# Optimization experiments

Hardware: AMD Instinct MI355X
Metric: run time of the kernel (lower is better)

## Reference

```python
import jax, jax.numpy as jnp
import numpy as np


def _ln(x, g, b, eps=1e-5):
    m = x.mean(-1, keepdims=True)
    v = ((x - m) ** 2).mean(-1, keepdims=True)
    return (x - m) / jnp.sqrt(v + eps) * g + b


def _conv(x, w, b, stride, pad, groups):
    # x: NCHW, w: OIHW (I = in_ch/groups)
    out = jax.lax.conv_general_dilated(
        x, w, (stride, stride), [(pad, pad), (pad, pad)],
        dimension_numbers=('NCHW', 'OIHW', 'NCHW'), feature_group_count=groups)
    return out + b[None, :, None, None]


def _gelu(x):
    return jax.nn.gelu(x, approximate=False)  # torch nn.GELU (exact erf)


def _forward(x, H, W, lpu_w, lpu_b, n1_g, n1_b, conv2d_w, conv2d_b, cn_g, cn_b,
             q_w, sr1_w, sr1_b, an1_g, an1_b, sr2_w, sr2_b, an2_g, an2_b,
             kv1_w, kv2_w, proj_w, proj_b, n2_g, n2_b,
             fc1_w, fc1_b, dw_w, dw_b, fc2_w, fc2_b):
    B, N, C = x.shape
    cd = C // 4          # conv_part_dim = 64
    ad = C - cd          # attn_part_dim = 192
    nh = 8
    hg = nh // 2         # heads per group
    hd = ad // nh        # head_dim = 24
    scale = hd ** -0.5
    # ---- LPU: depthwise 3x3 conv residual ----
    xi = x.transpose(0, 2, 1).reshape(B, C, H, W)
    xi = _conv(xi, lpu_w, lpu_b, 1, 1, C) + xi
    x = xi.reshape(B, C, N).transpose(0, 2, 1)
    # ---- Attention branch (pre-LN) ----
    y = _ln(x, n1_g, n1_b)
    cp, ap = y[..., :cd], y[..., cd:]
    # conv part: dense 3x3 conv (sr_ratio==8 -> kernel 3, pad 1), then LN+GELU in NLC
    cp = cp.reshape(B, H, W, cd).transpose(0, 3, 1, 2)
    cp = _conv(cp, conv2d_w, conv2d_b, 1, 1, 1).reshape(B, cd, N).transpose(0, 2, 1)
    cp = _gelu(_ln(cp, cn_g, cn_b))
    # attn part: dual spatial-reduction KV paths
    q = (ap @ q_w.T).reshape(B, N, nh, hd).transpose(0, 2, 1, 3)  # [B,nh,N,hd]
    x_ = ap.transpose(0, 2, 1).reshape(B, ad, H, W)
    x1 = _conv(x_, sr1_w, sr1_b, 8, 0, ad).reshape(B, ad, -1).transpose(0, 2, 1)  # [B,(H/8)(W/8),ad]
    x1 = _gelu(_ln(x1, an1_g, an1_b))
    x2 = _conv(x_, sr2_w, sr2_b, 4, 0, ad).reshape(B, ad, -1).transpose(0, 2, 1)  # [B,(H/4)(W/4),ad]
    x2 = _gelu(_ln(x2, an2_g, an2_b))
    kv1 = (x1 @ kv1_w.T).reshape(B, -1, 2, hg, hd).transpose(2, 0, 3, 1, 4)  # [2,B,hg,M1,hd]
    kv2 = (x2 @ kv2_w.T).reshape(B, -1, 2, hg, hd).transpose(2, 0, 3, 1, 4)

    def attn(qh, k, v):
        a = jax.nn.softmax(jnp.einsum('bhnd,bhmd->bhnm', qh, k) * scale, axis=-1)
        o = jnp.einsum('bhnm,bhmd->bhnd', a, v)
        return o.transpose(0, 2, 1, 3).reshape(B, N, -1)

    o1 = attn(q[:, :hg], kv1[0], kv1[1])
    o2 = attn(q[:, hg:], kv2[0], kv2[1])
    y = jnp.concatenate([o1, o2, cp], axis=-1) @ proj_w.T + proj_b
    x = x + y
    # ---- MLP with depthwise conv ----
    z = _ln(x, n2_g, n2_b) @ fc1_w.T + fc1_b
    hidc = z.shape[-1]
    z = z.transpose(0, 2, 1).reshape(B, hidc, H, W)
    z = _conv(z, dw_w, dw_b, 1, 1, hidc).reshape(B, hidc, N).transpose(0, 2, 1)
    z = _gelu(z) @ fc2_w.T + fc2_b
    return x + z


def setup_inputs() -> dict:
    key = jax.random.key(0)
    ks = jax.random.split(key, 16)
    B, H, W, C = 16, 56, 56, 256
    N = H * W
    cd, ad = C // 4, C * 3 // 4
    hid = 4 * C
    f = lambda i, shape, s=0.02: jax.random.normal(ks[i], shape, jnp.float32) * s
    return dict(
        x=jax.random.normal(ks[0], (B, N, C), jnp.float32),
        H=H, W=W,
        lpu_w=f(1, (C, 1, 3, 3), 0.1), lpu_b=jnp.zeros((C,), jnp.float32),
        n1_g=jnp.ones((C,), jnp.float32), n1_b=jnp.zeros((C,), jnp.float32),
        conv2d_w=f(2, (cd, cd, 3, 3), 0.05), conv2d_b=jnp.zeros((cd,), jnp.float32),
        cn_g=jnp.ones((cd,), jnp.float32), cn_b=jnp.zeros((cd,), jnp.float32),
        q_w=f(3, (ad, ad)),
        sr1_w=f(4, (ad, 1, 8, 8), 0.1), sr1_b=jnp.zeros((ad,), jnp.float32),
        an1_g=jnp.ones((ad,), jnp.float32), an1_b=jnp.zeros((ad,), jnp.float32),
        sr2_w=f(5, (ad, 1, 4, 4), 0.1), sr2_b=jnp.zeros((ad,), jnp.float32),
        an2_g=jnp.ones((ad,), jnp.float32), an2_b=jnp.zeros((ad,), jnp.float32),
        kv1_w=f(6, (ad, ad)), kv2_w=f(7, (ad, ad)),
        proj_w=f(8, (C, C)), proj_b=jnp.zeros((C,), jnp.float32),
        n2_g=jnp.ones((C,), jnp.float32), n2_b=jnp.zeros((C,), jnp.float32),
        fc1_w=f(9, (hid, C)), fc1_b=jnp.zeros((hid,), jnp.float32),
        dw_w=f(10, (hid, 1, 3, 3), 0.1), dw_b=jnp.zeros((hid,), jnp.float32),
        fc2_w=f(11, (C, hid)), fc2_b=jnp.zeros((C,), jnp.float32),
    )


def reference(x, H, W, lpu_w, lpu_b, n1_g, n1_b, conv2d_w, conv2d_b, cn_g, cn_b,
              q_w, sr1_w, sr1_b, an1_g, an1_b, sr2_w, sr2_b, an2_g, an2_b,
              kv1_w, kv2_w, proj_w, proj_b, n2_g, n2_b,
              fc1_w, fc1_b, dw_w, dw_b, fc2_w, fc2_b):
    return _forward(x, H, W, lpu_w, lpu_b, n1_g, n1_b, conv2d_w, conv2d_b, cn_g, cn_b,
                    q_w, sr1_w, sr1_b, an1_g, an1_b, sr2_w, sr2_b, an2_g, an2_b,
                    kv1_w, kv2_w, proj_w, proj_b, n2_g, n2_b,
                    fc1_w, fc1_b, dw_w, dw_b, fc2_w, fc2_b)
```

## Files before the change

kernel.cpp:

```cpp
#include <hip/hip_runtime.h>
#include <math.h>

#define BB   16
#define HH   56
#define WW   56
#define NN   (HH*WW)
#define CC   256
#define CD   64
#define AD   192
#define NH   8
#define HG   4
#define HD   24
#define HID  1024
#define M1   49
#define M2   196
#define BNR  (BB*NN)

typedef __attribute__((ext_vector_type(8))) short s8v;
typedef __attribute__((ext_vector_type(4))) short s4v;
typedef __attribute__((ext_vector_type(4))) float f4v;
typedef __attribute__((ext_vector_type(8))) _Float16 h8v;
typedef __attribute__((ext_vector_type(2))) _Float16 h2v;

__device__ __forceinline__ float gelu_f(float x) {
    float u = x * (1.0f + 0.044715f * x * x);
    float t = __expf(-1.5957691216f * u);
    return x * __builtin_amdgcn_rcpf(1.0f + t);
}
__device__ __forceinline__ ushort f2bf(float f) {
    union { float f; uint32_t u; } c; c.f = f;
    uint32_t u = c.u;
    return (ushort)((u + 0x7fffu + ((u >> 16) & 1u)) >> 16);
}
__device__ __forceinline__ float bf2f(ushort u) {
    union { uint32_t u; float f; } c; c.u = ((uint32_t)u) << 16;
    return c.f;
}
__device__ __forceinline__ ushort f2h(float f) {
    union { _Float16 h; ushort u; } c; c.h = (_Float16)f;
    return c.u;
}
__device__ __forceinline__ void load_lds16(const void* gsrc, void* ldst) {
    __builtin_amdgcn_global_load_lds(
        (const __attribute__((address_space(1))) void*)gsrc,
        (__attribute__((address_space(3))) void*)ldst, 16, 0, 0);
}
__device__ __forceinline__ int xcd_swz(int bid, int nwg) {
    int q = nwg >> 3, r = nwg & 7;
    int x = bid & 7, i = bid >> 3;
    return (x < r ? x * (q + 1) : r * (q + 1) + (x - r) * q) + i;
}

__global__ __launch_bounds__(256) void wprep_kernel(
        const float* __restrict__ qw, const float* __restrict__ k1,
        const float* __restrict__ k2, const float* __restrict__ pw,
        const float* __restrict__ f1, const float* __restrict__ f2,
        const float* __restrict__ cw, const float* __restrict__ lw,
        const float* __restrict__ dw,
        ushort* __restrict__ wq, ushort* __restrict__ wkv1,
        ushort* __restrict__ wkv2, ushort* __restrict__ wpr,
        ushort* __restrict__ wf1, ushort* __restrict__ wf2,
        ushort* __restrict__ wcp, float* __restrict__ lpwt,
        ushort* __restrict__ dwwth) {
    int i = blockIdx.x * 256 + threadIdx.x;
    if (i < 36864) { wq[i] = f2bf(qw[i]); return; } i -= 36864;
    if (i < 36864) { wkv1[i] = f2bf(k1[i]); return; } i -= 36864;
    if (i < 36864) { wkv2[i] = f2bf(k2[i]); return; } i -= 36864;
    if (i < 65536) { wpr[i] = f2bf(pw[i]); return; } i -= 65536;
    if (i < 262144) { wf1[i] = f2bf(f1[i]); return; } i -= 262144;
    if (i < 262144) { wf2[i] = f2h(f2[i]); return; } i -= 262144;
    if (i < 36864) {
        int co = i / 576, k = i - co * 576;
        int tap = k >> 6, ci = k & 63;
        wcp[i] = f2bf(cw[co * 576 + ci * 9 + tap]);
        return;
    } i -= 36864;
    if (i < 2304) { int c = i / 9, t = i - c * 9; lpwt[t * CC + c] = lw[i]; return; } i -= 2304;
    if (i < 9216) { int c = i / 9, t = i - c * 9; dwwth[t * HID + c] = f2h(dw[i]); }
}

__global__ __launch_bounds__(256) void lpu_kernel(const float* __restrict__ x,
        const float* __restrict__ wt, const float* __restrict__ bias,
        const float* __restrict__ n1g, const float* __restrict__ n1b,
        ushort* __restrict__ xbuf, ushort* __restrict__ ybuf) {
    int tid = threadIdx.x;
    int lane = tid & 63, wv = tid >> 6;
    int c = lane * 4;
    int grp = xcd_swz(blockIdx.x, NN / 16) * 4 + wv;
    int n0 = grp * 4;
    int h = n0 / WW, x0 = n0 - h * WW;
    int b = blockIdx.y;
    const float* xb = x + (size_t)b * NN * CC + c;
    float4 wreg[9];
#pragma unroll
    for (int t = 0; t < 9; ++t) wreg[t] = *(const float4*)(wt + t * CC + c);
    float4 bz = *(const float4*)(bias + c);
    float4 acc[4] = {bz, bz, bz, bz};
#pragma unroll
    for (int cx = 0; cx < 6; ++cx) {
        int wx = x0 + cx - 1;
        if ((unsigned)wx >= (unsigned)WW) continue;
#pragma unroll
        for (int ky = 0; ky < 3; ++ky) {
            int hy = h + ky - 1;
            if ((unsigned)hy >= (unsigned)HH) continue;
            float4 xv = *(const float4*)(xb + (size_t)(hy * WW + wx) * CC);
#pragma unroll
            for (int xo = 0; xo < 4; ++xo) {
                int kx = cx - xo;
                if (kx < 0 || kx > 2) continue;
                float4 wv4 = wreg[ky * 3 + kx];
                acc[xo].x = fmaf(xv.x, wv4.x, acc[xo].x);
                acc[xo].y = fmaf(xv.y, wv4.y, acc[xo].y);
                acc[xo].z = fmaf(xv.z, wv4.z, acc[xo].z);
                acc[xo].w = fmaf(xv.w, wv4.w, acc[xo].w);
            }
        }
    }
    float4 gv = *(const float4*)(n1g + c);
    float4 bv = *(const float4*)(n1b + c);
#pragma unroll
    for (int xo = 0; xo < 4; ++xo) {
        size_t o = ((size_t)b * NN + n0 + xo) * CC + c;
        float4 rv = *(const float4*)(x + o);
        float4 a = acc[xo];
        a.x += rv.x; a.y += rv.y; a.z += rv.z; a.w += rv.w;
        s4v xv4;
        xv4.x = (short)f2bf(a.x);
        xv4.y = (short)f2bf(a.y);
        xv4.z = (short)f2bf(a.z);
        xv4.w = (short)f2bf(a.w);
        *(s4v*)(xbuf + o) = xv4;
        float s = a.x + a.y + a.z + a.w;
        float sq = a.x * a.x + a.y * a.y + a.z * a.z + a.w * a.w;
#pragma unroll
        for (int off = 32; off >= 1; off >>= 1) {
            s += __shfl_xor(s, off, 64);
            sq += __shfl_xor(sq, off, 64);
        }
        float mean = s * (1.0f / 256.0f);
        float var = sq * (1.0f / 256.0f) - mean * mean;
        float rstd = rsqrtf(var + 1e-5f);
        s4v ov;
        ov.x = (short)f2bf((a.x - mean) * rstd * gv.x + bv.x);
        ov.y = (short)f2bf((a.y - mean) * rstd * gv.y + bv.y);
        ov.z = (short)f2bf((a.z - mean) * rstd * gv.z + bv.z);
        ov.w = (short)f2bf((a.w - mean) * rstd * gv.w + bv.w);
        *(s4v*)(ybuf + o) = ov;
    }
}

__device__ __forceinline__ void cpgemm_body(
        const ushort* __restrict__ y, const ushort* __restrict__ wt,
        const float* __restrict__ cb, const float* __restrict__ cng,
        const float* __restrict__ cnb, ushort* __restrict__ cat,
        ushort* As , ushort* Ws , int tile) {
    int tid = threadIdx.x;
    int wid = tid >> 6, lane = tid & 63;
    int rt = xcd_swz(tile, BNR / 128) * 128;
    int r0 = tid >> 2, c0 = tid & 3;
    int r1 = r0 + 64;
    int tok0 = rt + r0, tok1 = rt + r1;
    int b0 = tok0 / NN, n0 = tok0 - b0 * NN, h0 = n0 / WW, w0 = n0 - h0 * WW;
    int b1 = tok1 / NN, n1 = tok1 - b1 * NN, h1 = n1 / WW, w1 = n1 - h1 * WW;
    const ushort* Wp = wt + (size_t)r0 * 576 + c0 * 8;
    int aw0 = (c0 ^ (r0 & 3)) << 3;
    f4v acc[2][4];
#pragma unroll
    for (int m = 0; m < 2; ++m)
#pragma unroll
        for (int n = 0; n < 4; ++n) acc[m][n] = (f4v)0.f;
    int lr = lane & 15, g4 = lane >> 4;
    int swz = (g4 ^ (lr & 3)) << 3;
    for (int kt = 0; kt < 576; kt += 32) {
        int tap = kt >> 6, ci0 = kt & 63;
        int t3 = tap / 3, dy = t3 - 1, dx = (tap - t3 * 3) - 1;
        s8v a0 = (s8v)0, a1 = (s8v)0;
        int hy0 = h0 + dy, wx0 = w0 + dx;
        if ((unsigned)hy0 < (unsigned)HH && (unsigned)wx0 < (unsigned)WW)
            a0 = *(const s8v*)(y + ((size_t)b0 * NN + hy0 * WW + wx0) * CC + ci0 + c0 * 8);
        int hy1 = h1 + dy, wx1 = w1 + dx;
        if ((unsigned)hy1 < (unsigned)HH && (unsigned)wx1 < (unsigned)WW)
            a1 = *(const s8v*)(y + ((size_t)b1 * NN + hy1 * WW + wx1) * CC + ci0 + c0 * 8);
        s8v wv = *(const s8v*)(Wp + kt);
        __syncthreads();
        *(s8v*)&As[r0 * 32 + aw0] = a0;
        *(s8v*)&As[r1 * 32 + aw0] = a1;
        *(s8v*)&Ws[r0 * 32 + aw0] = wv;
        __syncthreads();
        s8v af[2], bf[4];
#pragma unroll
        for (int m = 0; m < 2; ++m)
            af[m] = *(const s8v*)&As[(wid * 32 + m * 16 + lr) * 32 + swz];
#pragma unroll
        for (int n = 0; n < 4; ++n)
            bf[n] = *(const s8v*)&Ws[(n * 16 + lr) * 32 + swz];
#pragma unroll
        for (int m = 0; m < 2; ++m)
#pragma unroll
            for (int n = 0; n < 4; ++n)
                acc[m][n] = __builtin_amdgcn_mfma_f32_16x16x32_bf16(af[m], bf[n], acc[m][n], 0, 0, 0);
    }
    float gv[4], bv[4], cbv[4];
#pragma unroll
    for (int n = 0; n < 4; ++n) {
        int gc = n * 16 + lr;
        cbv[n] = cb[gc];
        gv[n] = cng[gc];
        bv[n] = cnb[gc];
    }
#pragma unroll
    for (int m = 0; m < 2; ++m)
#pragma unroll
        for (int r = 0; r < 4; ++r) {
            float s = 0.f, sq = 0.f;
#pragma unroll
            for (int n = 0; n < 4; ++n) {
                float v = acc[m][n][r] + cbv[n];
                acc[m][n][r] = v;
                s += v; sq += v * v;
            }
#pragma unroll
            for (int off = 1; off < 16; off <<= 1) {
                s += __shfl_xor(s, off, 64);
                sq += __shfl_xor(sq, off, 64);
            }
            float mean = s * (1.0f / 64.0f);
            float var = sq * (1.0f / 64.0f) - mean * mean;
            float rstd = rsqrtf(var + 1e-5f);
            int row = rt + wid * 32 + m * 16 + g4 * 4 + r;
            ushort* op = cat + (size_t)row * CC + 192;
#pragma unroll
            for (int n = 0; n < 4; ++n) {
                float v = (acc[m][n][r] - mean) * rstd * gv[n] + bv[n];
                op[n * 16 + lr] = f2bf(gelu_f(v));
            }
        }
}

template <int KS, int OW>
__device__ __forceinline__ void sr_body(const ushort* __restrict__ yap,
        const float* __restrict__ w, const float* __restrict__ bias,
        const float* __restrict__ g, const float* __restrict__ bt,
        ushort* __restrict__ out, int m, int b) {
    int ch = threadIdx.x;
    int oh = m / OW, ow = m - oh * OW;
    const ushort* yb = yap + (size_t)b * NN * CC;
    float acc = bias[ch];
#pragma unroll
    for (int ky = 0; ky < KS; ++ky)
#pragma unroll
        for (int kx = 0; kx < KS; ++kx)
            acc = fmaf(bf2f(yb[(size_t)((oh * KS + ky) * WW + ow * KS + kx) * CC + ch]),
                       w[ch * KS * KS + ky * KS + kx], acc);
    __shared__ float red[2][3];
    float s = acc, sq = acc * acc;
#pragma unroll
    for (int off = 32; off >= 1; off >>= 1) {
        s += __shfl_xor(s, off, 64);
        sq += __shfl_xor(sq, off, 64);
    }
    int wv = threadIdx.x >> 6, lane = threadIdx.x & 63;
    if (lane == 0) { red[0][wv] = s; red[1][wv] = sq; }
    __syncthreads();
    s = red[0][0] + red[0][1] + red[0][2];
    sq = red[1][0] + red[1][1] + red[1][2];
    float mean = s * (1.0f / 192.0f);
    float var = sq * (1.0f / 192.0f) - mean * mean;
    float rstd = rsqrtf(var + 1e-5f);
    float v = (acc - mean) * rstd * g[ch] + bt[ch];
    out[((size_t)b * (OW * OW) + m) * AD + ch] = f2bf(gelu_f(v));
}

__global__ __launch_bounds__(192) void sr_both(const ushort* __restrict__ yap,
        const float* __restrict__ w1, const float* __restrict__ b1,
        const float* __restrict__ g1, const float* __restrict__ t1,
        ushort* __restrict__ o1,
        const float* __restrict__ w2, const float* __restrict__ b2,
        const float* __restrict__ g2, const float* __restrict__ t2,
        ushort* __restrict__ o2) {
    int b = blockIdx.y;
    if (blockIdx.x < M2) sr_body<4, 14>(yap, w2, b2, g2, t2, o2, blockIdx.x, b);
    else                 sr_body<8, 7>(yap, w1, b1, g1, t1, o1, blockIdx.x - M2, b);
}

template <int MODE, int F16>
__device__ __forceinline__ void gemm_body(
        const ushort* __restrict__ A, int lda,
        const ushort* __restrict__ W, int K, int O,
        const float* __restrict__ bias,
        const ushort* __restrict__ res, int ldr,
        void* __restrict__ Cout, int ldc, int R,
        int gx, int nwg, int bid) {
    __shared__ __align__(16) ushort As[2 * 256 * 32];
    __shared__ __align__(16) ushort Ws[2 * 128 * 32];
    int tid = threadIdx.x;
    int w8 = tid >> 6, lane = tid & 63;
    int wr = w8 >> 1, wc = w8 & 1;
    int swzb = xcd_swz(bid, nwg);
    int rt = (swzb / gx) * 256, ot = (swzb % gx) * 128;
    int r0 = tid >> 2, cslot = tid & 3;
    int csrc = (cslot ^ (r0 & 3)) * 8;
    const ushort* Ap0 = A + (size_t)min(rt + r0, R - 1) * lda + csrc;
    const ushort* Ap1 = A + (size_t)min(rt + r0 + 128, R - 1) * lda + csrc;
    const ushort* Wp0 = W + (size_t)min(ot + r0, O - 1) * K + csrc;
    char* lA0 = (char*)As + w8 * 1024;
    char* lA1 = (char*)As + 8192 + w8 * 1024;
    char* lW0 = (char*)Ws + w8 * 1024;
    f4v acc[4][4];
#pragma unroll
    for (int m = 0; m < 4; ++m)
#pragma unroll
        for (int n = 0; n < 4; ++n) acc[m][n] = (f4v)0.f;
    int lr = lane & 15;
    int swz = ((lane >> 4) ^ (lr & 3)) << 3;
    load_lds16(Ap0, lA0);
    load_lds16(Ap1, lA1);
    load_lds16(Wp0, lW0);
    __syncthreads();
    int cur = 0;
    for (int kt = 0; kt < K; kt += 32) {
        if (kt + 32 < K) {
            int pa = (cur ^ 1) * 16384, pw = (cur ^ 1) * 8192;
            load_lds16(Ap0 + kt + 32, lA0 + pa);
            load_lds16(Ap1 + kt + 32, lA1 + pa);
            load_lds16(Wp0 + kt + 32, lW0 + pw);
        }
        const ushort* Ab = As + cur * 8192;
        const ushort* Wb = Ws + cur * 4096;
        s8v af[4], bf[4];
#pragma unroll
        for (int m = 0; m < 4; ++m)
            af[m] = *(const s8v*)&Ab[(wr * 64 + m * 16 + lr) * 32 + swz];
#pragma unroll
        for (int n = 0; n < 4; ++n)
            bf[n] = *(const s8v*)&Wb[(wc * 64 + n * 16 + lr) * 32 + swz];
#pragma unroll
        for (int m = 0; m < 4; ++m)
#pragma unroll
            for (int n = 0; n < 4; ++n) {
                if (F16) {
                    h8v ah = *(const h8v*)&af[m];
                    h8v bh = *(const h8v*)&bf[n];
                    acc[m][n] = __builtin_amdgcn_mfma_f32_16x16x32_f16(ah, bh, acc[m][n], 0, 0, 0);
                } else {
                    acc[m][n] = __builtin_amdgcn_mfma_f32_16x16x32_bf16(af[m], bf[n], acc[m][n], 0, 0, 0);
                }
            }
        __syncthreads();
        cur ^= 1;
    }
#pragma unroll
    for (int m = 0; m < 4; ++m)
#pragma unroll
        for (int n = 0; n < 4; ++n) {
            int gr = rt + wr * 64 + m * 16 + (lane >> 4) * 4;
            int gc = ot + wc * 64 + n * 16 + (lane & 15);
            if (gc >= O) continue;
#pragma unroll
            for (int r = 0; r < 4; ++r) {
                int row = gr + r;
                if (row >= R) continue;
                float v = acc[m][n][r];
                if (MODE & 1) v += bias[gc];
                if (MODE & 2) v += bf2f(res[(size_t)row * ldr + gc]);
                if (MODE & 4)      ((ushort*)Cout)[(size_t)row * ldc + gc] = f2bf(v);
                else if (MODE & 8) ((ushort*)Cout)[(size_t)row * ldc + gc] = f2h(v);
                else               ((float*)Cout)[(size_t)row * ldc + gc] = v;
            }
        }
}

__global__ __launch_bounds__(512) void kvq_all(
        const ushort* __restrict__ yap, const ushort* __restrict__ wq,
        ushort* __restrict__ qbuf,
        const ushort* __restrict__ x1g, const ushort* __restrict__ wkv1,
        ushort* __restrict__ kv1b,
        const ushort* __restrict__ x2g, const ushort* __restrict__ wkv2,
        ushort* __restrict__ kv2b) {
    int bid = blockIdx.y * 2 + blockIdx.x;
    if (blockIdx.z == 0) {
        gemm_body<4, 0>(yap, CC, wq, AD, AD, nullptr, nullptr, 0,
                        qbuf, AD, BNR, 2, 392, bid);
    } else if (blockIdx.z == 1) {
        if (blockIdx.y >= 4) return;
        gemm_body<4, 0>(x1g, AD, wkv1, AD, AD, nullptr, nullptr, 0,
                        kv1b, AD, BB * M1, 2, 8, bid);
    } else {
        if (blockIdx.y >= 13) return;
        gemm_body<4, 0>(x2g, AD, wkv2, AD, AD, nullptr, nullptr, 0,
                        kv2b, AD, BB * M2, 2, 26, bid);
    }
}

template <int MODE, int F16 = 0>
__global__ __launch_bounds__(1024) void gemm_8ph(
        const ushort* __restrict__ A, int lda,
        const ushort* __restrict__ W, int K, int O,
        const float* __restrict__ bias,
        const ushort* __restrict__ res, int ldr,
        void* __restrict__ Cout, int ldc, int R) {
    __shared__ __align__(16) ushort Al[2 * 256 * 64];
    __shared__ __align__(16) ushort Wl[2 * 256 * 64];
    int tid = threadIdx.x;
    int w16 = tid >> 6, lane = tid & 63;
    int wr = w16 >> 2, wc = w16 & 3;
    int nwg = gridDim.x * gridDim.y;
    int swzb = xcd_swz(blockIdx.y * gridDim.x + blockIdx.x, nwg);
    int rt = (swzb / gridDim.x) * 256, ot = (swzb % gridDim.x) * 256;
    int lr = lane & 15, g4 = lane >> 4;
    int swz = (g4 ^ (lr & 3)) << 3;
    int ar0 = tid >> 2, sp0 = tid & 3;
    int cs0 = ((sp0 ^ (ar0 & 3)) << 3);
    const ushort* Ap0 = A + (size_t)(rt + ar0) * lda + cs0;
    const ushort* Wp0 = W + (size_t)(ot + ar0) * K + cs0;
    int d0 = w16 * 1024;
    f4v acc[4][4];
#pragma unroll
    for (int m = 0; m < 4; ++m)
#pragma unroll
        for (int n = 0; n < 4; ++n)
            acc[m][n] = (f4v)((MODE & 1) ? bias[ot + wc * 64 + n * 16 + lr] : 0.0f);
    auto STAGE = [&](int s) {
        int t = s >> 1, hf = s & 1;
        int boff = (t & 1) * 32768 + hf * 16384;
        int kc = t * 64 + hf * 32;
        load_lds16(Ap0 + kc, (char*)Al + boff + d0);
        load_lds16(Wp0 + kc, (char*)Wl + boff + d0);
    };
    int nS = K >> 5;
    STAGE(0); STAGE(1); STAGE(2);
    for (int s = 0; s < nS; ++s) {
        if (s < nS - 2)       asm volatile("s_waitcnt vmcnt(4)" ::: "memory");
        else if (s == nS - 2) asm volatile("s_waitcnt vmcnt(2)" ::: "memory");
        else                  asm volatile("s_waitcnt vmcnt(0)" ::: "memory");
        __builtin_amdgcn_s_barrier();
        __builtin_amdgcn_sched_barrier(0);
        if (s + 3 < nS) STAGE(s + 3);
        int uoff = ((s >> 1) & 1) * 16384 + (s & 1) * 8192;
        const ushort* Ab = Al + uoff;
        const ushort* Wb = Wl + uoff;
        s8v af[4], bf[4];
#pragma unroll
        for (int m = 0; m < 4; ++m)
            af[m] = *(const s8v*)&Ab[(wr * 64 + m * 16 + lr) * 32 + swz];
#pragma unroll
        for (int n = 0; n < 4; ++n)
            bf[n] = *(const s8v*)&Wb[(wc * 64 + n * 16 + lr) * 32 + swz];
        __builtin_amdgcn_s_setprio(1);
#pragma unroll
        for (int m = 0; m < 4; ++m)
#pragma unroll
            for (int n = 0; n < 4; ++n) {
                if (F16) {
                    h8v ah = *(const h8v*)&af[m];
                    h8v bh = *(const h8v*)&bf[n];
                    acc[m][n] = __builtin_amdgcn_mfma_f32_16x16x32_f16(ah, bh, acc[m][n], 0, 0, 0);
                } else {
                    acc[m][n] = __builtin_amdgcn_mfma_f32_16x16x32_bf16(af[m], bf[n], acc[m][n], 0, 0, 0);
                }
            }
        __builtin_amdgcn_s_setprio(0);
    }
#pragma unroll
    for (int m = 0; m < 4; ++m) {
        int gr = rt + wr * 64 + m * 16 + g4 * 4;
#pragma unroll
        for (int n = 0; n < 4; ++n) {
            int gc = ot + wc * 64 + n * 16 + lr;
#pragma unroll
            for (int r = 0; r < 4; ++r) {
                int row = gr + r;
                float v = acc[m][n][r];
                if (MODE & 2) v += bf2f(res[(size_t)row * ldr + gc]);
                if (MODE & 4)      ((ushort*)Cout)[(size_t)row * ldc + gc] = f2bf(v);
                else if (MODE & 8) ((ushort*)Cout)[(size_t)row * ldc + gc] = f2h(v);
                else               ((float*)Cout)[(size_t)row * ldc + gc] = v;
            }
        }
    }
}

__global__ __launch_bounds__(512) void projln_kernel(
        const ushort* __restrict__ A, const ushort* __restrict__ W,
        const float* __restrict__ bias,
        const float* __restrict__ n2g, const float* __restrict__ n2b,
        ushort* __restrict__ xbuf, ushort* __restrict__ ybuf) {
    __shared__ __align__(16) ushort As[128 * 32];
    __shared__ __align__(16) ushort Ws[256 * 32];
    int tid = threadIdx.x;
    int w8 = tid >> 6, lane = tid & 63;
    int rt = xcd_swz(blockIdx.x, BNR / 128) * 128;
    int r0 = tid >> 2, cslot = tid & 3;
    int csrc = (cslot ^ (r0 & 3)) * 8;
    const ushort* Ap0 = A + (size_t)(rt + r0) * CC + csrc;
    const ushort* Wp0 = W + (size_t)r0 * CC + csrc;
    const ushort* Wp1 = W + (size_t)(r0 + 128) * CC + csrc;
    char* lA0 = (char*)As + w8 * 1024;
    char* lW0 = (char*)Ws + w8 * 1024;
    char* lW1 = (char*)Ws + 8192 + w8 * 1024;
    int lr = lane & 15, g4 = lane >> 4;
    int swz = (g4 ^ (lr & 3)) << 3;
    f4v acc[16];
#pragma unroll
    for (int n = 0; n < 16; ++n) acc[n] = (f4v)(bias[n * 16 + lr]);
    for (int kt = 0; kt < CC; kt += 32) {
        __syncthreads();
        load_lds16(Ap0 + kt, lA0);
        load_lds16(Wp0 + kt, lW0);
        load_lds16(Wp1 + kt, lW1);
        __syncthreads();
        s8v af = *(const s8v*)&As[(w8 * 16 + lr) * 32 + swz];
#pragma unroll
        for (int n = 0; n < 16; ++n) {
            s8v bf = *(const s8v*)&Ws[(n * 16 + lr) * 32 + swz];
            acc[n] = __builtin_amdgcn_mfma_f32_16x16x32_bf16(af, bf, acc[n], 0, 0, 0);
        }
    }
#pragma unroll
    for (int r = 0; r < 4; ++r) {
        int row = rt + w8 * 16 + g4 * 4 + r;
        ushort* xr = xbuf + (size_t)row * CC;
        ushort* yr = ybuf + (size_t)row * CC;
        float s = 0.f, sq = 0.f;
#pragma unroll
        for (int n = 0; n < 16; ++n) {
            float v = acc[n][r] + bf2f(xr[n * 16 + lr]);
            acc[n][r] = v;
            s += v; sq += v * v;
        }
#pragma unroll
        for (int off = 1; off < 16; off <<= 1) {
            s += __shfl_xor(s, off, 64);
            sq += __shfl_xor(sq, off, 64);
        }
        float mean = s * (1.0f / 256.0f);
        float var = sq * (1.0f / 256.0f) - mean * mean;
        float rstd = rsqrtf(var + 1e-5f);
#pragma unroll
        for (int n = 0; n < 16; ++n) {
            int col = n * 16 + lr;
            float v = acc[n][r];
            xr[col] = f2bf(v);
            yr[col] = f2bf((v - mean) * rstd * n2g[col] + n2b[col]);
        }
    }
}

template <int M, int MP>
__device__ __forceinline__ void attn_body(const ushort* __restrict__ q,
        const ushort* __restrict__ kvb, ushort* __restrict__ cat,
        ushort* Kl, ushort* VT, int g, int h, int b) {
    constexpr int NT = MP / 16;
    constexpr int NCH = MP / 32;
    int tid = threadIdx.x;
    for (int i = tid; i < MP * 4; i += 256) ((s8v*)Kl)[i] = (s8v)0;
    for (int i = tid; i < MP * 4; i += 256) ((s8v*)VT)[i] = (s8v)0;
    __syncthreads();
    for (int u = tid; u < M * 3; u += 256) {
        int m = u / 3, d0 = u - m * 3;
        s8v kv8 = *(const s8v*)(kvb + ((size_t)b * M + m) * AD + g * HD + d0 * 8);
        *(s8v*)&Kl[m * 32 + ((d0 ^ (m & 3)) << 3)] = kv8;
    }
    for (int u = tid; u < M * 3; u += 256) {
        int m = u / 3, d0 = u - m * 3;
        s8v vv = *(const s8v*)(kvb + ((size_t)b * M + m) * AD + 96 + g * HD + d0 * 8);
        int c = m >> 5, mm = m & 31;
        int gg = (mm >> 2) & 3;
        int t = (mm & 3) + ((mm & 16) >> 2);
#pragma unroll
        for (int j = 0; j < 8; ++j) {
            int d = d0 * 8 + j;
            VT[d * MP + ((c * 4 + (gg ^ (d & 3))) << 3) + t] = (ushort)vv[j];
        }
    }
    __syncthreads();
    int w = tid >> 6, lane = tid & 63;
    int ln = lane & 15, g4 = lane >> 4;
    int swz = (g4 ^ (ln & 3)) << 3;
    const float scale = 0.20412414523193154f;
    for (int nt = 0; nt < 4; ++nt) {
        int nbase = blockIdx.x * 256 + nt * 64;
        if (nbase >= NN) break;
        int n0 = nbase + w * 16 + ln;
        s8v qf = (s8v)0;
        if (g4 < 3) qf = *(const s8v*)(q + ((size_t)b * NN + n0) * AD + h * HD + g4 * 8);
        f4v sa[NT];
#pragma unroll
        for (int t = 0; t < NT; ++t) sa[t] = (f4v)0.f;
#pragma unroll
        for (int t = 0; t < NT; ++t) {
            s8v kf = *(const s8v*)&Kl[(t * 16 + ln) * 32 + swz];
            sa[t] = __builtin_amdgcn_mfma_f32_16x16x32_bf16(kf, qf, sa[t], 0, 0, 0);
        }
        float mx = -3.0e38f;
#pragma unroll
        for (int t = 0; t < NT; ++t)
#pragma unroll
            for (int r = 0; r < 4; ++r) {
                int m = t * 16 + g4 * 4 + r;
                float v = (m < M) ? sa[t][r] * scale : -3.0e38f;
                sa[t][r] = v;
                mx = fmaxf(mx, v);
            }
        mx = fmaxf(mx, __shfl_xor(mx, 16, 64));
        mx = fmaxf(mx, __shfl_xor(mx, 32, 64));
        float sum = 0.f;
#pragma unroll
        for (int t = 0; t < NT; ++t)
#pragma unroll
            for (int r = 0; r < 4; ++r) {
                float p = __expf(sa[t][r] - mx);
                sa[t][r] = p;
                sum += p;
            }
        sum += __shfl_xor(sum, 16, 64);
        sum += __shfl_xor(sum, 32, 64);
        float inv = 1.0f / sum;
        f4v oa[2] = {(f4v)0.f, (f4v)0.f};
#pragma unroll
        for (int c = 0; c < NCH; ++c) {
            s8v pb;
#pragma unroll
            for (int t = 0; t < 4; ++t) {
                pb[t]     = (short)f2bf(sa[c * 2][t]);
                pb[4 + t] = (short)f2bf(sa[c * 2 + 1][t]);
            }
#pragma unroll
            for (int dt = 0; dt < 2; ++dt) {
                s8v vf = *(const s8v*)&VT[(dt * 16 + ln) * MP + c * 32 + swz];
                oa[dt] = __builtin_amdgcn_mfma_f32_16x16x32_bf16(vf, pb, oa[dt], 0, 0, 0);
            }
        }
        ushort* op = cat + ((size_t)b * NN + n0) * CC + h * HD;
        s4v o0;
#pragma unroll
        for (int r = 0; r < 4; ++r) o0[r] = (short)f2bf(oa[0][r] * inv);
        *(s4v*)(op + g4 * 4) = o0;
        if (g4 < 2) {
            s4v o1;
#pragma unroll
            for (int r = 0; r < 4; ++r) o1[r] = (short)f2bf(oa[1][r] * inv);
            *(s4v*)(op + 16 + g4 * 4) = o1;
        }
    }
}

__global__ __launch_bounds__(256) void attn_both(const ushort* __restrict__ q,
        const ushort* __restrict__ kv1b, const ushort* __restrict__ kv2b,
        ushort* __restrict__ cat,
        const ushort* __restrict__ ybuf, const ushort* __restrict__ wcp,
        const float* __restrict__ cb, const float* __restrict__ cng,
        const float* __restrict__ cnb) {
    __shared__ __align__(16) ushort Kl[224 * 32];
    __shared__ __align__(16) ushort VT[32 * 224];
    int hy = blockIdx.y, b = blockIdx.z;
    if (hy < HG)      attn_body<M1, 64>(q, kv1b, cat, Kl, VT, hy, hy, b);
    else if (hy < NH) attn_body<M2, 224>(q, kv2b, cat, Kl, VT, hy - HG, hy, b);
    else {
        int id = blockIdx.x + 13 * blockIdx.z;
        for (int t = id * 2; t < id * 2 + 2; ++t)
            if (t < BNR / 128)
                cpgemm_body(ybuf, wcp, cb, cng, cnb, cat, Kl, VT, t);
    }
}

__global__ __launch_bounds__(256) void dwconv_kernel(const ushort* __restrict__ z1,
        const ushort* __restrict__ wt, const float* __restrict__ bias,
        ushort* __restrict__ z2) {
    int bid = xcd_swz(blockIdx.x, HH * 7);
    int h = bid / 7, bx = bid - h * 7;
    int b = blockIdx.y;
    int c = (threadIdx.x & 127) * 8;
    int x0 = bx * 8 + (threadIdx.x >> 7) * 4;
    const ushort* zrow = z1 + ((size_t)b * NN + h * WW) * HID + c;
    h2v wreg[9][4];
#pragma unroll
    for (int t = 0; t < 9; ++t) {
        s8v w8 = *(const s8v*)(wt + t * HID + c);
        const h2v* wp = (const h2v*)&w8;
#pragma unroll
        for (int p = 0; p < 4; ++p) wreg[t][p] = wp[p];
    }
    h2v acc[4][4];
    {
        float4 b0 = *(const float4*)(bias + c);
        float4 b1 = *(const float4*)(bias + c + 4);
        h2v bz[4];
        bz[0][0] = (_Float16)b0.x; bz[0][1] = (_Float16)b0.y;
        bz[1][0] = (_Float16)b0.z; bz[1][1] = (_Float16)b0.w;
        bz[2][0] = (_Float16)b1.x; bz[2][1] = (_Float16)b1.y;
        bz[3][0] = (_Float16)b1.z; bz[3][1] = (_Float16)b1.w;
#pragma unroll
        for (int xo = 0; xo < 4; ++xo)
#pragma unroll
            for (int p = 0; p < 4; ++p) acc[xo][p] = bz[p];
    }
#pragma unroll
    for (int cx = 0; cx < 6; ++cx) {
        int wx = x0 + cx - 1;
        if ((unsigned)wx >= (unsigned)WW) continue;
#pragma unroll
        for (int ky = 0; ky < 3; ++ky) {
            int hy = h + ky - 1;
            if ((unsigned)hy >= (unsigned)HH) continue;
            s8v v = *(const s8v*)(zrow + ((size_t)(ky - 1) * WW + wx) * HID);
            const h2v* v2 = (const h2v*)&v;
#pragma unroll
            for (int xo = 0; xo < 4; ++xo) {
                int kx = cx - xo;
                if (kx < 0 || kx > 2) continue;
#pragma unroll
                for (int p = 0; p < 4; ++p)
                    acc[xo][p] = v2[p] * wreg[ky * 3 + kx][p] + acc[xo][p];
            }
        }
    }
    ushort* zo = z2 + ((size_t)b * NN + h * WW + x0) * HID + c;
#pragma unroll
    for (int xo = 0; xo < 4; ++xo) {
        s8v o;
#pragma unroll
        for (int p = 0; p < 4; ++p) {
            o[p * 2]     = (short)f2h(gelu_f((float)acc[xo][p][0]));
            o[p * 2 + 1] = (short)f2h(gelu_f((float)acc[xo][p][1]));
        }
        *(s8v*)(zo + (size_t)xo * HID) = o;
    }
}

extern "C" void kernel_launch(void* const* d_in, const int* in_sizes, int n_in,
                              void* d_out, int out_size, void* d_ws, size_t ws_size,
                              hipStream_t stream) {
    const float* x      = (const float*)d_in[0];
    const float* lpu_w  = (const float*)d_in[3];
    const float* lpu_b  = (const float*)d_in[4];
    const float* n1_g   = (const float*)d_in[5];
    const float* n1_b   = (const float*)d_in[6];
    const float* c2_w   = (const float*)d_in[7];
    const float* c2_b   = (const float*)d_in[8];
    const float* cn_g   = (const float*)d_in[9];
    const float* cn_b   = (const float*)d_in[10];
    const float* q_w    = (const float*)d_in[11];
    const float* sr1_w  = (const float*)d_in[12];
    const float* sr1_b  = (const float*)d_in[13];
    const float* an1_g  = (const float*)d_in[14];
    const float* an1_b  = (const float*)d_in[15];
    const float* sr2_w  = (const float*)d_in[16];
    const float* sr2_b  = (const float*)d_in[17];
    const float* an2_g  = (const float*)d_in[18];
    const float* an2_b  = (const float*)d_in[19];
    const float* kv1_w  = (const float*)d_in[20];
    const float* kv2_w  = (const float*)d_in[21];
    const float* proj_w = (const float*)d_in[22];
    const float* proj_b = (const float*)d_in[23];
    const float* n2_g   = (const float*)d_in[24];
    const float* n2_b   = (const float*)d_in[25];
    const float* fc1_w  = (const float*)d_in[26];
    const float* fc1_b  = (const float*)d_in[27];
    const float* dw_w   = (const float*)d_in[28];
    const float* dw_b   = (const float*)d_in[29];
    const float* fc2_w  = (const float*)d_in[30];
    const float* fc2_b  = (const float*)d_in[31];
    float* out = (float*)d_out;

    char* ws = (char*)d_ws;
    size_t off = 0;
    auto allocB = [&](size_t bytes) {
        char* p = ws + off;
        off += ((bytes + 255) & ~(size_t)255);
        return p;
    };
    ushort* xbuf = (ushort*)allocB((size_t)BNR * CC * 2);
    ushort* ybuf = (ushort*)allocB((size_t)BNR * CC * 2);
    ushort* wq   = (ushort*)allocB((size_t)AD * AD * 2);
    ushort* wkv1 = (ushort*)allocB((size_t)AD * AD * 2);
    ushort* wkv2 = (ushort*)allocB((size_t)AD * AD * 2);
    ushort* wpr  = (ushort*)allocB((size_t)CC * CC * 2);
    ushort* wf1  = (ushort*)allocB((size_t)HID * CC * 2);
    ushort* wf2  = (ushort*)allocB((size_t)CC * HID * 2);
    ushort* wcp  = (ushort*)allocB((size_t)64 * 576 * 2);
    float*  lpwt = (float*)allocB((size_t)9 * CC * 4);
    ushort* dwwt = (ushort*)allocB((size_t)9 * HID * 2);
    size_t zmark = off;
    ushort* cat  = (ushort*)allocB((size_t)BNR * CC * 2);
    ushort* qbuf = (ushort*)allocB((size_t)BNR * AD * 2);
    ushort* x1g  = (ushort*)allocB((size_t)BB * M1 * AD * 2);
    ushort* x2g  = (ushort*)allocB((size_t)BB * M2 * AD * 2);
    ushort* kv1b = (ushort*)allocB((size_t)BB * M1 * AD * 2);
    ushort* kv2b = (ushort*)allocB((size_t)BB * M2 * AD * 2);

    int CB2 = 1;
    for (int cb = 16; cb >= 1; cb >>= 1) {
        if (zmark + 2 * (size_t)cb * NN * HID * 2 <= ws_size) { CB2 = cb; break; }
    }

    dim3 b256(256), b512(512), b1024(1024);
    wprep_kernel<<<dim3(2925), b256, 0, stream>>>(
        q_w, kv1_w, kv2_w, proj_w, fc1_w, fc2_w, c2_w, lpu_w, dw_w,
        wq, wkv1, wkv2, wpr, wf1, wf2, wcp, lpwt, dwwt);
    lpu_kernel<<<dim3(NN / 16, BB), b256, 0, stream>>>(x, lpwt, lpu_b, n1_g, n1_b, xbuf, ybuf);
    sr_both<<<dim3(M1 + M2, BB), dim3(192), 0, stream>>>(ybuf + CD,
        sr1_w, sr1_b, an1_g, an1_b, x1g, sr2_w, sr2_b, an2_g, an2_b, x2g);
    kvq_all<<<dim3(2, 196, 3), b512, 0, stream>>>(
        ybuf + CD, wq, qbuf, x1g, wkv1, kv1b, x2g, wkv2, kv2b);
    attn_both<<<dim3((NN + 255) / 256, NH + 1, BB), b256, 0, stream>>>(
        qbuf, kv1b, kv2b, cat, ybuf, wcp, c2_b, cn_g, cn_b);
    projln_kernel<<<dim3(BNR / 128), b512, 0, stream>>>(
        cat, wpr, proj_b, n2_g, n2_b, xbuf, ybuf);
    ushort* z1 = (ushort*)(ws + zmark);
    ushort* z2 = z1 + (size_t)CB2 * NN * HID;
    for (int c0 = 0; c0 < BB; c0 += CB2) {
        size_t tokoff = (size_t)c0 * NN;
        int Rr = CB2 * NN;
        gemm_8ph<9><<<dim3(HID / 256, Rr / 256), b1024, 0, stream>>>(
            ybuf + tokoff * CC, CC, wf1, CC, HID, fc1_b, nullptr, 0, z1, HID, Rr);
        dwconv_kernel<<<dim3(HH * 7, CB2), b256, 0, stream>>>(z1, dwwt, dw_b, z2);
        gemm_8ph<3, 1><<<dim3(CC / 256, Rr / 256), b1024, 0, stream>>>(
            z2, HID, wf2, HID, CC, fc2_b, xbuf + tokoff * CC, CC, out + tokoff * CC, CC, Rr);
    }
}
```

Before: 332.4 us.

## Shrink MLP GEMM tiles to 128x256 with 512 threads and double-buffered K

Changes the FC1/FC2 GEMM kernel from a 256x256 tile run by 1024 threads to a 128x256 tile run by 512 threads. LDS use drops to two 32-wide K stages, and launch bounds allow four blocks per CU. The triple-staged prefetch is replaced by double buffering with an extra barrier before each refill. The aim is more concurrent blocks and better load balance, because NN*CB2 rows divide more evenly into 128-row tiles. The cost is less operand reuse per tile and an extra barrier per K step.

```diff
diff --git a/kernel.cpp b/kernel.cpp
--- a/kernel.cpp
+++ b/kernel.cpp
@@ -394,27 +394,28 @@
 }
 
 template <int MODE, int F16 = 0>
-__global__ __launch_bounds__(1024) void gemm_8ph(
+__global__ __launch_bounds__(512, 4) void gemm_8ph(
         const ushort* __restrict__ A, int lda,
         const ushort* __restrict__ W, int K, int O,
         const float* __restrict__ bias,
         const ushort* __restrict__ res, int ldr,
         void* __restrict__ Cout, int ldc, int R) {
-    __shared__ __align__(16) ushort Al[2 * 256 * 64];
-    __shared__ __align__(16) ushort Wl[2 * 256 * 64];
+    __shared__ __align__(16) ushort Al[2 * 128 * 32];
+    __shared__ __align__(16) ushort Wl[2 * 256 * 32];
     int tid = threadIdx.x;
-    int w16 = tid >> 6, lane = tid & 63;
-    int wr = w16 >> 2, wc = w16 & 3;
+    int w8 = tid >> 6, lane = tid & 63;
+    int wr = w8 >> 2, wc = w8 & 3;
     int nwg = gridDim.x * gridDim.y;
     int swzb = xcd_swz(blockIdx.y * gridDim.x + blockIdx.x, nwg);
-    int rt = (swzb / gridDim.x) * 256, ot = (swzb % gridDim.x) * 256;
+    int rt = (swzb / gridDim.x) * 128, ot = (swzb % gridDim.x) * 256;
     int lr = lane & 15, g4 = lane >> 4;
     int swz = (g4 ^ (lr & 3)) << 3;
     int ar0 = tid >> 2, sp0 = tid & 3;
     int cs0 = ((sp0 ^ (ar0 & 3)) << 3);
     const ushort* Ap0 = A + (size_t)(rt + ar0) * lda + cs0;
     const ushort* Wp0 = W + (size_t)(ot + ar0) * K + cs0;
-    int d0 = w16 * 1024;
+    const ushort* Wp1 = W + (size_t)(ot + ar0 + 128) * K + cs0;
+    int d0 = w8 * 1024;
     f4v acc[4][4];
 #pragma unroll
     for (int m = 0; m < 4; ++m)
@@ -422,24 +423,21 @@
         for (int n = 0; n < 4; ++n)
             acc[m][n] = (f4v)((MODE & 1) ? bias[ot + wc * 64 + n * 16 + lr] : 0.0f);
     auto STAGE = [&](int s) {
-        int t = s >> 1, hf = s & 1;
-        int boff = (t & 1) * 32768 + hf * 16384;
-        int kc = t * 64 + hf * 32;
-        load_lds16(Ap0 + kc, (char*)Al + boff + d0);
-        load_lds16(Wp0 + kc, (char*)Wl + boff + d0);
+        int bo = s & 1;
+        int kc = s * 32;
+        load_lds16(Ap0 + kc, (char*)Al + bo * 8192 + d0);
+        load_lds16(Wp0 + kc, (char*)Wl + bo * 16384 + d0);
+        load_lds16(Wp1 + kc, (char*)Wl + bo * 16384 + 8192 + d0);
     };
     int nS = K >> 5;
-    STAGE(0); STAGE(1); STAGE(2);
+    STAGE(0); STAGE(1);
     for (int s = 0; s < nS; ++s) {
-        if (s < nS - 2)       asm volatile("s_waitcnt vmcnt(4)" ::: "memory");
-        else if (s == nS - 2) asm volatile("s_waitcnt vmcnt(2)" ::: "memory");
-        else                  asm volatile("s_waitcnt vmcnt(0)" ::: "memory");
+        if (s == nS - 1) asm volatile("s_waitcnt vmcnt(0)" ::: "memory");
+        else             asm volatile("s_waitcnt vmcnt(3)" ::: "memory");
         __builtin_amdgcn_s_barrier();
         __builtin_amdgcn_sched_barrier(0);
-        if (s + 3 < nS) STAGE(s + 3);
-        int uoff = ((s >> 1) & 1) * 16384 + (s & 1) * 8192;
-        const ushort* Ab = Al + uoff;
-        const ushort* Wb = Wl + uoff;
+        const ushort* Ab = Al + (s & 1) * 4096;
+        const ushort* Wb = Wl + (s & 1) * 8192;
         s8v af[4], bf[4];
 #pragma unroll
         for (int m = 0; m < 4; ++m)
@@ -461,6 +459,8 @@
                 }
             }
         __builtin_amdgcn_s_setprio(0);
+        __builtin_amdgcn_s_barrier();
+        if (s + 2 < nS) STAGE(s + 2);
     }
 #pragma unroll
     for (int m = 0; m < 4; ++m) {
@@ -795,7 +795,7 @@
         if (zmark + 2 * (size_t)cb * NN * HID * 2 <= ws_size) { CB2 = cb; break; }
     }
 
-    dim3 b256(256), b512(512), b1024(1024);
+    dim3 b256(256), b512(512);
     wprep_kernel<<<dim3(2925), b256, 0, stream>>>(
         q_w, kv1_w, kv2_w, proj_w, fc1_w, fc2_w, c2_w, lpu_w, dw_w,
         wq, wkv1, wkv2, wpr, wf1, wf2, wcp, lpwt, dwwt);
@@ -813,10 +813,10 @@
     for (int c0 = 0; c0 < BB; c0 += CB2) {
         size_t tokoff = (size_t)c0 * NN;
         int Rr = CB2 * NN;
-        gemm_8ph<9><<<dim3(HID / 256, Rr / 256), b1024, 0, stream>>>(
+        gemm_8ph<9><<<dim3(HID / 256, Rr / 128), b512, 0, stream>>>(
             ybuf + tokoff * CC, CC, wf1, CC, HID, fc1_b, nullptr, 0, z1, HID, Rr);
         dwconv_kernel<<<dim3(HH * 7, CB2), b256, 0, stream>>>(z1, dwwt, dw_b, z2);
-        gemm_8ph<3, 1><<<dim3(CC / 256, Rr / 256), b1024, 0, stream>>>(
+        gemm_8ph<3, 1><<<dim3(CC / 256, Rr / 128), b512, 0, stream>>>(
             z2, HID, wf2, HID, CC, fc2_b, xbuf + tokoff * CC, CC, out + tokoff * CC, CC, Rr);
     }
 }
```

New measurement: 333.3 us. No clear change (+0.3%).
